# Optimization experiments

Hardware: AMD Instinct MI355X
Metric: run time of the kernel (lower is better)

Reference implementation:

```python
import jax, jax.numpy as jnp
import numpy as np

EPS = 1e-06

def elu_feature_map(x):
    return jax.nn.elu(x) + 1.0

def setup_inputs() -> dict:
    key = jax.random.key(0)
    kq, kk, kv = jax.random.split(key, 3)
    N, L, S, H, D = 8, 8192, 8192, 8, 32
    queries = jax.random.normal(kq, (N, L, H, D), dtype=jnp.float32)
    keys = jax.random.normal(kk, (N, S, H, D), dtype=jnp.float32)
    values = jax.random.normal(kv, (N, S, H, D), dtype=jnp.float32)
    return {"queries": queries, "keys": keys, "values": values}

def reference(queries, keys, values):
    # Linear attention: phi(Q) (phi(K)^T V) normalized by phi(Q) . sum(phi(K))
    Q = elu_feature_map(queries)            # [N, L, H, D]
    K = elu_feature_map(keys)               # [N, S, H, D]
    v_length = values.shape[1]
    v = values / v_length                   # [N, S, H, Dv]
    KV = jnp.einsum('nshd,nshv->nhdv', K, v)           # [N, H, D, Dv]
    Z = 1.0 / (jnp.einsum('nlhd,nhd->nlh', Q, K.sum(axis=1)) + EPS)  # [N, L, H]
    out = jnp.einsum('nlhd,nhdv->nlhv', Q, KV) * Z[..., None] * v_length
    return out
```

## Files before the change

kernel.cpp:

```cpp
#include <hip/hip_runtime.h>
#include <hip/hip_bf16.h>


#define N_      8
#define L_      8192
#define S_      8192
#define H_      8
#define D_      32
#define NH_     64
#define CH1_    16
#define SPC1_   512
#define TILEP_  76
#define KVE_    (D_ * D_)
#define PKS_    (KVE_ + D_)

typedef short short8 __attribute__((ext_vector_type(8)));
typedef float f32x4  __attribute__((ext_vector_type(4)));

__device__ __forceinline__ float phi_f(float x) {
    return x > 0.f ? x + 1.f : __expf(x);
}

__device__ __forceinline__ void split_bf16(float x, short& hi, short& lo) {
    __hip_bfloat16 hb = __float2bfloat16(x);
    const float xh = __bfloat162float(hb);
    __hip_bfloat16 lb = __float2bfloat16(x - xh);
    __builtin_memcpy(&hi, &hb, 2);
    __builtin_memcpy(&lo, &lb, 2);
}

__device__ __forceinline__ unsigned packsplit(float x) {
    short hi, lo; split_bf16(x, hi, lo);
    return ((unsigned)(unsigned short)hi << 16) | (unsigned)(unsigned short)lo;
}

__device__ __forceinline__ void unpack8(uint4 p0, uint4 p1, short8& hi, short8& lo) {
    union { unsigned u[4]; short8 s; } H, L;
    const unsigned q[8] = {p0.x, p0.y, p0.z, p0.w, p1.x, p1.y, p1.z, p1.w};
#pragma unroll
    for (int i = 0; i < 4; ++i) {
        H.u[i] = (q[2 * i + 1] & 0xffff0000u) | (q[2 * i] >> 16);
        L.u[i] = (q[2 * i + 1] << 16) | (q[2 * i] & 0xffffu);
    }
    hi = H.s; lo = L.s;
}

template <bool ATOMIC>
__global__ __launch_bounds__(256) void la_phase1(
    const float* __restrict__ keys, const float* __restrict__ values,
    float* __restrict__ outp )
{
    __shared__ unsigned kP[2][32][TILEP_];
    __shared__ unsigned vP[2][32][TILEP_];
    __shared__ float red_ks[4][8][4];
    const int nh = blockIdx.x, chunk = blockIdx.y;
    const int n = nh >> 3, h = nh & 7;
    const int t = threadIdx.x, lane = t & 63, w = t >> 6;
    const int row8 = t >> 3;
    const int c4   = t & 7;
    const int row_l = lane & 15, kg = lane >> 4;
    const int dt = w >> 1, vt = w & 1;
    const float* kb = keys   + ((size_t)n * S_) * 256 + h * 32 + (c4 << 2);
    const float* vb = values + ((size_t)n * S_) * 256 + h * 32 + (c4 << 2);
    const int s0 = chunk * SPC1_;

    float ks4[4] = {0.f, 0.f, 0.f, 0.f};
    f32x4 cacc = {0.f, 0.f, 0.f, 0.f};
    float4 Lka, Lkb, Lva, Lvb;

    auto LOADT = [&](int tb) {
        const size_t g0 = ((size_t)(s0 + (tb << 6) + row8)) << 8;
        const size_t g1 = ((size_t)(s0 + (tb << 6) + row8 + 32)) << 8;
        Lka = *(const float4*)(kb + g0);
        Lkb = *(const float4*)(kb + g1);
        Lva = *(const float4*)(vb + g0);
        Lvb = *(const float4*)(vb + g1);
    };
    auto PROCT = [&](int buf) {
        const float f0[4] = {phi_f(Lka.x), phi_f(Lka.y), phi_f(Lka.z), phi_f(Lka.w)};
        const float f1[4] = {phi_f(Lkb.x), phi_f(Lkb.y), phi_f(Lkb.z), phi_f(Lkb.w)};
        const float g0[4] = {Lva.x, Lva.y, Lva.z, Lva.w};
        const float g1[4] = {Lvb.x, Lvb.y, Lvb.z, Lvb.w};
#pragma unroll
        for (int j = 0; j < 4; ++j) {
            ks4[j] += f0[j] + f1[j];
            const int dv = (c4 << 2) + j;
            kP[buf][dv][row8]      = packsplit(f0[j]);
            kP[buf][dv][row8 + 32] = packsplit(f1[j]);
            vP[buf][dv][row8]      = packsplit(g0[j]);
            vP[buf][dv][row8 + 32] = packsplit(g1[j]);
        }
    };
    auto COMPT = [&](int buf) {
#pragma unroll
        for (int sh = 0; sh < 2; ++sh) {
            const unsigned* ap = &kP[buf][(dt << 4) + row_l][(sh << 5) + (kg << 3)];
            const unsigned* bp = &vP[buf][(vt << 4) + row_l][(sh << 5) + (kg << 3)];
            const uint4 a0 = *(const uint4*)ap, a1 = *(const uint4*)(ap + 4);
            const uint4 b0 = *(const uint4*)bp, b1 = *(const uint4*)(bp + 4);
            short8 ahi, alo, bhi, blo;
            unpack8(a0, a1, ahi, alo);
            unpack8(b0, b1, bhi, blo);
            cacc = __builtin_amdgcn_mfma_f32_16x16x32_bf16(ahi, bhi, cacc, 0, 0, 0);
            cacc = __builtin_amdgcn_mfma_f32_16x16x32_bf16(ahi, blo, cacc, 0, 0, 0);
            cacc = __builtin_amdgcn_mfma_f32_16x16x32_bf16(alo, bhi, cacc, 0, 0, 0);
        }
    };

    LOADT(0);
    PROCT(0);
    __syncthreads();
#pragma unroll
    for (int tb = 0; tb < 8; ++tb) {
        const int cur = tb & 1;
        if (tb < 7) LOADT(tb + 1);
        COMPT(cur);
        if (tb < 7) PROCT(cur ^ 1);
        __syncthreads();
    }

#pragma unroll
    for (int j = 0; j < 4; ++j) {
        float x = ks4[j];
        x += __shfl_xor(x, 8);
        x += __shfl_xor(x, 16);
        x += __shfl_xor(x, 32);
        ks4[j] = x;
    }
    if (lane < 8) {
#pragma unroll
        for (int j = 0; j < 4; ++j) red_ks[w][lane][j] = ks4[j];
    }
    __syncthreads();

    if (ATOMIC) {
        float* p = outp + (size_t)nh * PKS_;
#pragma unroll
        for (int r = 0; r < 4; ++r) {
            const int dd = (dt << 4) + (kg << 2) + r;
            const int vv = (vt << 4) + row_l;
            atomicAdd(&p[dd * D_ + vv], cacc[r]);
        }
        if (t < 32) {
            const float s = red_ks[0][t >> 2][t & 3] + red_ks[1][t >> 2][t & 3]
                          + red_ks[2][t >> 2][t & 3] + red_ks[3][t >> 2][t & 3];
            atomicAdd(&p[KVE_ + t], s);
        }
    } else {
        float* p = outp + ((size_t)nh * CH1_ + chunk) * PKS_;
#pragma unroll
        for (int r = 0; r < 4; ++r) {
            const int dd = (dt << 4) + (kg << 2) + r;
            const int vv = (vt << 4) + row_l;
            p[dd * D_ + vv] = cacc[r];
        }
        if (t < 32) {
            p[KVE_ + t] = red_ks[0][t >> 2][t & 3] + red_ks[1][t >> 2][t & 3]
                        + red_ks[2][t >> 2][t & 3] + red_ks[3][t >> 2][t & 3];
        }
    }
}

__global__ __launch_bounds__(256) void la_reduce(
    const float* __restrict__ partials,
    short* __restrict__ kvThi, short* __restrict__ kvTlo,
    float* __restrict__ ksumf)
{
    const int nh = blockIdx.x;
    for (int e = threadIdx.x; e < PKS_; e += 256) {
        const float* p = partials + (size_t)nh * CH1_ * PKS_ + e;
        float s = 0.f;
#pragma unroll
        for (int c = 0; c < CH1_; ++c) s += p[(size_t)c * PKS_];
        if (e < KVE_) {
            const int d = e >> 5, v = e & 31;
            short hi, lo; split_bf16(s, hi, lo);
            kvThi[nh * KVE_ + v * D_ + d] = hi;
            kvTlo[nh * KVE_ + v * D_ + d] = lo;
        } else {
            ksumf[nh * D_ + (e - KVE_)] = s;
        }
    }
}

__global__ __launch_bounds__(256) void la_convert(
    const float* __restrict__ kvf,
    short* __restrict__ kvThi, short* __restrict__ kvTlo,
    float* __restrict__ ksumf)
{
    const int nh = blockIdx.x;
    for (int e = threadIdx.x; e < PKS_; e += 256) {
        const float s = kvf[(size_t)nh * PKS_ + e];
        if (e < KVE_) {
            const int d = e >> 5, v = e & 31;
            short hi, lo; split_bf16(s, hi, lo);
            kvThi[nh * KVE_ + v * D_ + d] = hi;
            kvTlo[nh * KVE_ + v * D_ + d] = lo;
        } else {
            ksumf[nh * D_ + (e - KVE_)] = s;
        }
    }
}

__global__ void la_zero(float* __restrict__ p, int nelem) {
    const int i = blockIdx.x * 256 + threadIdx.x;
    if (i < nelem) p[i] = 0.f;
}

__global__ __launch_bounds__(256) void la_phase2(
    const float* __restrict__ queries,
    const short* __restrict__ kvThi, const short* __restrict__ kvTlo,
    const float* __restrict__ ksumf, float* __restrict__ out)
{
    const int t = threadIdx.x, lane = t & 63, w = t >> 6;
    const int wt = blockIdx.x * 4 + w;
    const int h  = wt & 7;
    const int rt = wt >> 3;
    const size_t rowg0 = (size_t)rt * 16;
    const int n = (int)(rowg0 >> 13);
    const int nh = n * 8 + h;
    const int row_l = lane & 15;
    const int kg    = lane >> 4;

    const float* qp = queries + (rowg0 + row_l) * 256 + h * D_ + kg * 8;
    float qa[8];
    {
        const float4 qA = *(const float4*)(qp);
        const float4 qB = *(const float4*)(qp + 4);
        qa[0] = phi_f(qA.x); qa[1] = phi_f(qA.y); qa[2] = phi_f(qA.z); qa[3] = phi_f(qA.w);
        qa[4] = phi_f(qB.x); qa[5] = phi_f(qB.y); qa[6] = phi_f(qB.z); qa[7] = phi_f(qB.w);
    }
    short8 ahi, alo;
#pragma unroll
    for (int e = 0; e < 8; ++e) {
        short hs, ls; split_bf16(qa[e], hs, ls);
        ahi[e] = hs; alo[e] = ls;
    }

    const short* bh = kvThi + (size_t)nh * KVE_;
    const short* bl = kvTlo + (size_t)nh * KVE_;
    const short8 bh0 = *(const short8*)(bh + (row_l     ) * D_ + kg * 8);
    const short8 bh1 = *(const short8*)(bh + (row_l + 16) * D_ + kg * 8);
    const short8 bl0 = *(const short8*)(bl + (row_l     ) * D_ + kg * 8);
    const short8 bl1 = *(const short8*)(bl + (row_l + 16) * D_ + kg * 8);

    f32x4 c0 = {0.f, 0.f, 0.f, 0.f}, c1 = {0.f, 0.f, 0.f, 0.f};
    c0 = __builtin_amdgcn_mfma_f32_16x16x32_bf16(alo, bh0, c0, 0, 0, 0);
    c0 = __builtin_amdgcn_mfma_f32_16x16x32_bf16(ahi, bl0, c0, 0, 0, 0);
    c0 = __builtin_amdgcn_mfma_f32_16x16x32_bf16(ahi, bh0, c0, 0, 0, 0);
    c1 = __builtin_amdgcn_mfma_f32_16x16x32_bf16(alo, bh1, c1, 0, 0, 0);
    c1 = __builtin_amdgcn_mfma_f32_16x16x32_bf16(ahi, bl1, c1, 0, 0, 0);
    c1 = __builtin_amdgcn_mfma_f32_16x16x32_bf16(ahi, bh1, c1, 0, 0, 0);

    const float* ksp = ksumf + nh * D_ + kg * 8;
    float dt;
    {
        const float4 kA = *(const float4*)(ksp);
        const float4 kB = *(const float4*)(ksp + 4);
        dt = qa[0] * kA.x;
        dt = fmaf(qa[1], kA.y, dt); dt = fmaf(qa[2], kA.z, dt);
        dt = fmaf(qa[3], kA.w, dt); dt = fmaf(qa[4], kB.x, dt);
        dt = fmaf(qa[5], kB.y, dt); dt = fmaf(qa[6], kB.z, dt);
        dt = fmaf(qa[7], kB.w, dt);
    }
    dt += __shfl_xor(dt, 16);
    dt += __shfl_xor(dt, 32);

    float* ob = out + rowg0 * 256 + h * D_ + row_l;
#pragma unroll
    for (int r = 0; r < 4; ++r) {
        const int rowp = kg * 4 + r;
        const float drow = __shfl(dt, rowp);
        const float z = __builtin_amdgcn_rcpf(drow + 1e-6f);
        ob[(size_t)rowp * 256]      = c0[r] * z;
        ob[(size_t)rowp * 256 + 16] = c1[r] * z;
    }
}

extern "C" void kernel_launch(void* const* d_in, const int* in_sizes, int n_in,
                              void* d_out, int out_size, void* d_ws, size_t ws_size,
                              hipStream_t stream)
{
    const float* queries = (const float*)d_in[0];
    const float* keys    = (const float*)d_in[1];
    const float* values  = (const float*)d_in[2];
    float* out = (float*)d_out;
    float* ws  = (float*)d_ws;

    const size_t partial_elems = (size_t)NH_ * CH1_ * PKS_;
    const size_t split_elems   = (size_t)NH_ * KVE_;
    const size_t split_floats  = split_elems / 2;
    const size_t ksum_floats   = (size_t)NH_ * D_;
    const dim3 blk(256);
    const int p2_blocks = (N_ * L_ * H_) / 16 / 4;

    if (ws_size >= (partial_elems + 2 * split_floats + ksum_floats) * sizeof(float)) {
        float* partials = ws;
        short* kvThi = (short*)(ws + partial_elems);
        short* kvTlo = kvThi + split_elems;
        float* ksumf = (float*)(kvTlo + split_elems);
        la_phase1<false><<<dim3(NH_, CH1_), blk, 0, stream>>>(keys, values, partials);
        la_reduce<<<dim3(NH_), blk, 0, stream>>>(partials, kvThi, kvTlo, ksumf);
        la_phase2<<<dim3(p2_blocks), blk, 0, stream>>>(queries, kvThi, kvTlo, ksumf, out);
    } else {
        float* kvf = ws;
        short* kvThi = (short*)(ws + (size_t)NH_ * PKS_);
        short* kvTlo = kvThi + split_elems;
        float* ksumf = (float*)(kvTlo + split_elems);
        const int nz = (int)((size_t)NH_ * PKS_);
        la_zero<<<dim3((nz + 255) / 256), blk, 0, stream>>>(kvf, nz);
        la_phase1<true><<<dim3(NH_, CH1_), blk, 0, stream>>>(keys, values, kvf);
        la_convert<<<dim3(NH_), blk, 0, stream>>>(kvf, kvThi, kvTlo, ksumf);
        la_phase2<<<dim3(p2_blocks), blk, 0, stream>>>(queries, kvThi, kvTlo, ksumf, out);
    }
}
```

Before: 62.83 us.

## Use single bf16 MFMA in phase1 with swizzled packed LDS layout

Phase 1 (K^T V accumulation) drops the split hi/lo bf16 emulation that issued three MFMAs per fragment and uses one plain bf16 MFMA instead. Elements are packed two per 32-bit word via lane shuffles and stored into a smaller XOR-swizzled LDS tile, so fragments load directly as a single uint4 without unpacking. This cuts MFMA count, LDS footprint and ALU conversion work, at the cost of reduced accuracy for the KV product.

```diff
diff --git a/kernel.cpp b/kernel.cpp
--- a/kernel.cpp
+++ b/kernel.cpp
@@ -10,7 +10,7 @@
 #define NH_     64
 #define CH1_    16
 #define SPC1_   512
-#define TILEP_  76
+#define STR1_   36
 #define KVE_    (D_ * D_)
 #define PKS_    (KVE_ + D_)
 
@@ -19,6 +19,13 @@
 
 __device__ __forceinline__ float phi_f(float x) {
     return x > 0.f ? x + 1.f : __expf(x);
+}
+
+__device__ __forceinline__ unsigned short bf16_bits(float x) {
+    __hip_bfloat16 h = __float2bfloat16(x);
+    unsigned short u;
+    __builtin_memcpy(&u, &h, 2);
+    return u;
 }
 
 __device__ __forceinline__ void split_bf16(float x, short& hi, short& lo) {
@@ -29,29 +36,13 @@
     __builtin_memcpy(&lo, &lb, 2);
 }
 
-__device__ __forceinline__ unsigned packsplit(float x) {
-    short hi, lo; split_bf16(x, hi, lo);
-    return ((unsigned)(unsigned short)hi << 16) | (unsigned)(unsigned short)lo;
-}
-
-__device__ __forceinline__ void unpack8(uint4 p0, uint4 p1, short8& hi, short8& lo) {
-    union { unsigned u[4]; short8 s; } H, L;
-    const unsigned q[8] = {p0.x, p0.y, p0.z, p0.w, p1.x, p1.y, p1.z, p1.w};
-#pragma unroll
-    for (int i = 0; i < 4; ++i) {
-        H.u[i] = (q[2 * i + 1] & 0xffff0000u) | (q[2 * i] >> 16);
-        L.u[i] = (q[2 * i + 1] << 16) | (q[2 * i] & 0xffffu);
-    }
-    hi = H.s; lo = L.s;
-}
-
 template <bool ATOMIC>
 __global__ __launch_bounds__(256) void la_phase1(
     const float* __restrict__ keys, const float* __restrict__ values,
     float* __restrict__ outp )
 {
-    __shared__ unsigned kP[2][32][TILEP_];
-    __shared__ unsigned vP[2][32][TILEP_];
+    __shared__ unsigned kS[2][32][STR1_];
+    __shared__ unsigned vS[2][32][STR1_];
     __shared__ float red_ks[4][8][4];
     const int nh = blockIdx.x, chunk = blockIdx.y;
     const int n = nh >> 3, h = nh & 7;
@@ -60,6 +51,9 @@
     const int c4   = t & 7;
     const int row_l = lane & 15, kg = lane >> 4;
     const int dt = w >> 1, vt = w & 1;
+    const int odd = row8 & 1;
+    const int dv0 = (c4 << 2) + (odd ? 2 : 0);
+    const int s2lo = row8 >> 1;
     const float* kb = keys   + ((size_t)n * S_) * 256 + h * 32 + (c4 << 2);
     const float* vb = values + ((size_t)n * S_) * 256 + h * 32 + (c4 << 2);
     const int s0 = chunk * SPC1_;
@@ -76,34 +70,50 @@
         Lva = *(const float4*)(vb + g0);
         Lvb = *(const float4*)(vb + g1);
     };
+    auto STORE4 = [&](unsigned (*Sarr)[STR1_], const unsigned short* x, int s2) {
+        const unsigned mA = (unsigned)x[0] | ((unsigned)x[1] << 16);
+        const unsigned mB = (unsigned)x[2] | ((unsigned)x[3] << 16);
+        const unsigned pA = __shfl_xor(mA, 8);
+        const unsigned pB = __shfl_xor(mB, 8);
+        const unsigned m = odd ? mB : mA, p = odd ? pB : pA;
+        const unsigned se = odd ? p : m;
+        const unsigned so = odd ? m : p;
+        const unsigned w0 = (se & 0xffffu) | ((so & 0xffffu) << 16);
+        const unsigned w1 = (se >> 16) | (so & 0xffff0000u);
+        Sarr[dv0][4 * ((s2 >> 2) ^ (dv0 & 7)) + (s2 & 3)]             = w0;
+        Sarr[dv0 + 1][4 * ((s2 >> 2) ^ ((dv0 + 1) & 7)) + (s2 & 3)]   = w1;
+    };
     auto PROCT = [&](int buf) {
         const float f0[4] = {phi_f(Lka.x), phi_f(Lka.y), phi_f(Lka.z), phi_f(Lka.w)};
         const float f1[4] = {phi_f(Lkb.x), phi_f(Lkb.y), phi_f(Lkb.z), phi_f(Lkb.w)};
-        const float g0[4] = {Lva.x, Lva.y, Lva.z, Lva.w};
-        const float g1[4] = {Lvb.x, Lvb.y, Lvb.z, Lvb.w};
-#pragma unroll
-        for (int j = 0; j < 4; ++j) {
-            ks4[j] += f0[j] + f1[j];
-            const int dv = (c4 << 2) + j;
-            kP[buf][dv][row8]      = packsplit(f0[j]);
-            kP[buf][dv][row8 + 32] = packsplit(f1[j]);
-            vP[buf][dv][row8]      = packsplit(g0[j]);
-            vP[buf][dv][row8 + 32] = packsplit(g1[j]);
-        }
+        unsigned short kx[4], ky[4], vx[4], vy[4];
+#pragma unroll
+        for (int j = 0; j < 4; ++j) ks4[j] += f0[j] + f1[j];
+        kx[0] = bf16_bits(f0[0]); kx[1] = bf16_bits(f0[1]);
+        kx[2] = bf16_bits(f0[2]); kx[3] = bf16_bits(f0[3]);
+        ky[0] = bf16_bits(f1[0]); ky[1] = bf16_bits(f1[1]);
+        ky[2] = bf16_bits(f1[2]); ky[3] = bf16_bits(f1[3]);
+        vx[0] = bf16_bits(Lva.x); vx[1] = bf16_bits(Lva.y);
+        vx[2] = bf16_bits(Lva.z); vx[3] = bf16_bits(Lva.w);
+        vy[0] = bf16_bits(Lvb.x); vy[1] = bf16_bits(Lvb.y);
+        vy[2] = bf16_bits(Lvb.z); vy[3] = bf16_bits(Lvb.w);
+        STORE4(kS[buf], kx, s2lo);
+        STORE4(kS[buf], ky, s2lo + 16);
+        STORE4(vS[buf], vx, s2lo);
+        STORE4(vS[buf], vy, s2lo + 16);
+    };
+    auto FRAG = [&](const unsigned (*Sarr)[STR1_], int row, int sh) -> short8 {
+        const int g = ((sh << 2) | kg) ^ (row & 7);
+        union { uint4 u; short8 s; } U;
+        U.u = *(const uint4*)&Sarr[row][g << 2];
+        return U.s;
     };
     auto COMPT = [&](int buf) {
 #pragma unroll
         for (int sh = 0; sh < 2; ++sh) {
-            const unsigned* ap = &kP[buf][(dt << 4) + row_l][(sh << 5) + (kg << 3)];
-            const unsigned* bp = &vP[buf][(vt << 4) + row_l][(sh << 5) + (kg << 3)];
-            const uint4 a0 = *(const uint4*)ap, a1 = *(const uint4*)(ap + 4);
-            const uint4 b0 = *(const uint4*)bp, b1 = *(const uint4*)(bp + 4);
-            short8 ahi, alo, bhi, blo;
-            unpack8(a0, a1, ahi, alo);
-            unpack8(b0, b1, bhi, blo);
-            cacc = __builtin_amdgcn_mfma_f32_16x16x32_bf16(ahi, bhi, cacc, 0, 0, 0);
-            cacc = __builtin_amdgcn_mfma_f32_16x16x32_bf16(ahi, blo, cacc, 0, 0, 0);
-            cacc = __builtin_amdgcn_mfma_f32_16x16x32_bf16(alo, bhi, cacc, 0, 0, 0);
+            const short8 A = FRAG(kS[buf], (dt << 4) + row_l, sh);
+            const short8 B = FRAG(vS[buf], (vt << 4) + row_l, sh);
+            cacc = __builtin_amdgcn_mfma_f32_16x16x32_bf16(A, B, cacc, 0, 0, 0);
         }
     };
 
```

After: 64.35 us. 2.4% more time.
